# Kernel optimization log

Measured on AMD Instinct MI355X. Metric: run time of the kernel, lower is better.

The kernel has to match this reference:

```python
import jax, jax.numpy as jnp
import numpy as np

H = 4      # num_attention_heads
DK = 75    # d_k = hidden_size // H
HID = 300  # hidden_size


def setup_inputs() -> dict:
    key = jax.random.key(0)
    ks = jax.random.split(key, 9)
    B, S = 8, 2048
    query = jax.random.normal(ks[0], (B, S, HID), dtype=jnp.float32)
    key_t = jax.random.normal(ks[1], (B, S, HID), dtype=jnp.float32)
    value = jax.random.normal(ks[2], (B, S, HID), dtype=jnp.float32)
    mask = jax.random.randint(ks[3], (B, S), 0, 2, dtype=jnp.int32)
    scale = 1.0 / np.sqrt(HID)
    Wq = jax.random.normal(ks[4], (HID, HID), dtype=jnp.float32) * scale
    Wk = jax.random.normal(ks[5], (HID, HID), dtype=jnp.float32) * scale
    Wv = jax.random.normal(ks[6], (HID, HID), dtype=jnp.float32) * scale
    Wo = jax.random.normal(ks[7], (HID, HID), dtype=jnp.float32) * scale
    bo = jax.random.normal(ks[8], (HID,), dtype=jnp.float32) * 0.01
    return {"query": query, "key": key_t, "value": value, "mask": mask,
            "Wq": Wq, "Wk": Wk, "Wv": Wv, "Wo": Wo, "bo": bo}


def reference(query, key, value, mask, Wq, Wk, Wv, Wo, bo):
    B, S, _ = query.shape
    # QKV projections (nn.Linear: x @ W.T), split into heads: [B,H,S,DK]
    def proj(x, W):
        return (x @ W.T).reshape(B, S, H, DK).transpose(0, 2, 1, 3)
    q, k, v = proj(query, Wq), proj(key, Wk), proj(value, Wv)
    # scores: [B,H,S,S]
    scores = jnp.einsum('bhqd,bhkd->bhqk', q, k) / jnp.sqrt(jnp.float32(DK))
    # mask outer product 'bi,bj->bij' broadcast over heads; fill zeros with -1e9
    m2 = (mask[:, :, None] * mask[:, None, :])[:, None, :, :]  # [B,1,S,S]
    scores = jnp.where(m2 == 0, jnp.float32(-1e9), scores)
    p_attn = jax.nn.softmax(scores, axis=-1)  # dropout p=0.0 (eval mode)
    x = jnp.einsum('bhqk,bhkd->bhqd', p_attn, v)  # [B,H,S,DK]
    x = x.transpose(0, 2, 1, 3).reshape(B, S, H * DK)
    return x @ Wo.T + bo
```

## Files before the change

### kernel.cpp

```cpp
#include <hip/hip_runtime.h>
#include <math.h>

typedef __bf16 bf16x8 __attribute__((ext_vector_type(8)));
typedef float f32x4 __attribute__((ext_vector_type(4)));
typedef float f32x16 __attribute__((ext_vector_type(16)));
typedef unsigned short u16;
typedef u16 u16x8 __attribute__((ext_vector_type(8)));

#define HID 300
#define NH 4
#define DK 75
#define DKP 80
#define BB 8
#define SS 2048
#define BSROWS (BB*SS)
#define C2   0.16658807f

#define MFMA(a,b,c)   __builtin_amdgcn_mfma_f32_16x16x32_bf16(a,b,c,0,0,0)
#define MFMA32(a,b,c) __builtin_amdgcn_mfma_f32_32x32x16_bf16(a,b,c,0,0,0)

static __device__ __forceinline__ void split2(float x, u16& hb, u16& lb) {
    const unsigned u = __float_as_uint(x);
    hb = (u16)(u >> 16);
    const float r = x - __uint_as_float(u & 0xffff0000u);
    lb = (u16)(__float_as_uint(r) >> 16);
}
static __device__ __forceinline__ void split2rne(float x, u16& hb, u16& lb) {
    const unsigned u = __float_as_uint(x);
    const unsigned uh = ((u + 0x7fffu + ((u >> 16) & 1u)) >> 16) << 16;
    hb = (u16)(uh >> 16);
    const float r = x - __uint_as_float(uh);
    lb = (u16)(__float_as_uint(r) >> 16);
}
static __device__ __forceinline__ unsigned pkbf(float a, float b) {
    const unsigned short ua = __builtin_bit_cast(unsigned short, (__bf16)a);
    const unsigned short ub = __builtin_bit_cast(unsigned short, (__bf16)b);
    return (unsigned)ua | ((unsigned)ub << 16);
}

__global__ __launch_bounds__(256)
void prep_w3(const float* __restrict__ Wq, const float* __restrict__ Wk,
             const float* __restrict__ Wv,
             u16* __restrict__ wph, u16* __restrict__ wpl)
{
    const int idx = blockIdx.x * 256 + threadIdx.x;
    if (idx >= 38400) return;
    const int c8 = idx % 40;
    int r = idx / 40;
    const int n = r % 80; r /= 80;
    const int h = r & 3;  r >>= 2;
    const int mat = r;
    const float* W = (mat == 0) ? Wq : (mat == 1) ? Wk : Wv;
    const int col0 = c8 * 8;
    float v[8];
#pragma unroll
    for (int j = 0; j < 8; ++j) v[j] = 0.f;
    if (n < DK) {
        const float* s = W + (size_t)(h * DK + n) * HID + col0;
        if (col0 + 8 <= HID) {
#pragma unroll
            for (int j = 0; j < 8; ++j) v[j] = s[j];
        } else {
#pragma unroll
            for (int j = 0; j < 8; ++j) v[j] = (col0 + j < HID) ? s[j] : 0.f;
        }
    }
    u16x8 hv, lv;
#pragma unroll
    for (int j = 0; j < 8; ++j) {
        u16 hb, lb;
        split2(v[j], hb, lb);
        hv[j] = hb; lv[j] = lb;
    }
    const size_t base = ((size_t)((mat * 4 + h) * 80 + n)) * 320 + col0;
    *(u16x8*)(wph + base) = hv;
    *(u16x8*)(wpl + base) = lv;
}

static __device__ __forceinline__ void gemm_body(
    char* smem, const float* __restrict__ A, const float* __restrict__ W,
    const u16* __restrict__ Wph, const u16* __restrict__ Wpl,
    const float* __restrict__ bias, u16* __restrict__ hiP, u16* __restrict__ loP,
    float* __restrict__ foutP, const int mode, const int bx, const int h,
    const int* __restrict__ pmask, const float scale, const int patch)
{
    u16* Ah = (u16*)smem;
    u16* Al = Ah + 128 * 40;
    u16* Wh = Al + 128 * 40;
    u16* Wl = Wh + 80 * 40;

    const int t = threadIdx.x;
    const int wv = t >> 6, l = t & 63, qc = l & 15, g = l >> 4;
    const int row0 = bx * 128;
    const int b = row0 >> 11;
    const int s0 = row0 & 2047;

    const f32x4 zf = {0.f, 0.f, 0.f, 0.f};
    f32x4 acc[2][5];
#pragma unroll
    for (int mt = 0; mt < 2; ++mt)
#pragma unroll
        for (int nt = 0; nt < 5; ++nt) acc[mt][nt] = zf;

    const int rA = t >> 1, halfA = t & 1;
    float4 aPf[4];
    u16x8 wPfH[2], wPfL[2];
    float4 wPf2[3];

    auto loadA = [&](int step) {
        const int k0 = step * 32 + halfA * 16;
        const float* src = A + (size_t)(row0 + rA) * HID + k0;
#pragma unroll
        for (int c4 = 0; c4 < 4; ++c4) {
            const int k = k0 + c4 * 4;
            float4 v;
            if (k + 4 <= HID) v = *(const float4*)(src + c4 * 4);
            else {
                v.x = (k + 0 < HID) ? src[c4 * 4 + 0] : 0.f;
                v.y = (k + 1 < HID) ? src[c4 * 4 + 1] : 0.f;
                v.z = (k + 2 < HID) ? src[c4 * 4 + 2] : 0.f;
                v.w = (k + 3 < HID) ? src[c4 * 4 + 3] : 0.f;
            }
            aPf[c4] = v;
        }
    };
    auto loadW = [&](int step) {
        const int k0 = step * 32;
        if (mode <= 1) {
#pragma unroll
            for (int j = 0; j < 2; ++j) {
                const int idx = j * 256 + t;
                if (idx < 320) {
                    const int n = idx >> 2, c = idx & 3;
                    const size_t wo = (size_t)(h * 80 + n) * 320 + k0 + c * 8;
                    wPfH[j] = *(const u16x8*)(Wph + wo);
                    wPfL[j] = *(const u16x8*)(Wpl + wo);
                }
            }
        } else {
#pragma unroll
            for (int j = 0; j < 3; ++j) {
                const int idx = j * 256 + t;
                if (idx < 640) {
                    const int n = idx >> 3, c = idx & 7;
                    const int k = k0 + c * 4;
                    float4 v = make_float4(0.f, 0.f, 0.f, 0.f);
                    if (n < DK) {
                        const float* src = W + (size_t)(h * DK + n) * HID + k;
                        if (k + 4 <= HID) v = *(const float4*)src;
                        else {
                            v.x = (k + 0 < HID) ? src[0] : 0.f;
                            v.y = (k + 1 < HID) ? src[1] : 0.f;
                            v.z = (k + 2 < HID) ? src[2] : 0.f;
                            v.w = (k + 3 < HID) ? src[3] : 0.f;
                        }
                    }
                    wPf2[j] = v;
                }
            }
        }
    };
    auto writeA = [&]() {
        u16* dh = Ah + rA * 40 + halfA * 16;
        u16* dl = Al + rA * 40 + halfA * 16;
#pragma unroll
        for (int c4 = 0; c4 < 4; ++c4) {
            ushort4 h4, l4;
            split2(aPf[c4].x, h4.x, l4.x);
            split2(aPf[c4].y, h4.y, l4.y);
            split2(aPf[c4].z, h4.z, l4.z);
            split2(aPf[c4].w, h4.w, l4.w);
            *(ushort4*)(dh + c4 * 4) = h4;
            *(ushort4*)(dl + c4 * 4) = l4;
        }
    };
    auto writeW = [&]() {
        if (mode <= 1) {
#pragma unroll
            for (int j = 0; j < 2; ++j) {
                const int idx = j * 256 + t;
                if (idx < 320) {
                    const int n = idx >> 2, c = idx & 3;
                    *(u16x8*)(Wh + n * 40 + c * 8) = wPfH[j];
                    *(u16x8*)(Wl + n * 40 + c * 8) = wPfL[j];
                }
            }
        } else {
#pragma unroll
            for (int j = 0; j < 3; ++j) {
                const int idx = j * 256 + t;
                if (idx < 640) {
                    const int n = idx >> 3, c = idx & 7;
                    ushort4 h4, l4;
                    split2(wPf2[j].x, h4.x, l4.x);
                    split2(wPf2[j].y, h4.y, l4.y);
                    split2(wPf2[j].z, h4.z, l4.z);
                    split2(wPf2[j].w, h4.w, l4.w);
                    *(ushort4*)(Wh + n * 40 + c * 4) = h4;
                    *(ushort4*)(Wl + n * 40 + c * 4) = l4;
                }
            }
        }
    };

    loadA(0);
    loadW(0);

    for (int step = 0; step < 10; ++step) {
        __syncthreads();
        writeA();
        writeW();
        __syncthreads();
        if (step < 9) {
            loadA(step + 1);
            loadW(step + 1);
        }
        bf16x8 ah[2], al2[2];
#pragma unroll
        for (int mt = 0; mt < 2; ++mt) {
            const int roff = (wv * 32 + mt * 16 + qc) * 40 + g * 8;
            ah[mt]  = *(const bf16x8*)(Ah + roff);
            al2[mt] = *(const bf16x8*)(Al + roff);
        }
#pragma unroll
        for (int nt = 0; nt < 5; ++nt) {
            const int woff = (nt * 16 + qc) * 40 + g * 8;
            const bf16x8 bh = *(const bf16x8*)(Wh + woff);
            const bf16x8 bl = *(const bf16x8*)(Wl + woff);
#pragma unroll
            for (int mt = 0; mt < 2; ++mt) {
                acc[mt][nt] = MFMA(ah[mt],  bh, acc[mt][nt]);
                acc[mt][nt] = MFMA(al2[mt], bh, acc[mt][nt]);
                acc[mt][nt] = MFMA(ah[mt],  bl, acc[mt][nt]);
            }
        }
    }
    __syncthreads();

    if (mode <= 1) {
        unsigned* epi = (unsigned*)smem;
#pragma unroll
        for (int mt = 0; mt < 2; ++mt)
#pragma unroll
            for (int nt = 0; nt < 5; ++nt)
#pragma unroll
                for (int r = 0; r < 4; ++r) {
                    u16 hb, lb;
                    split2rne(acc[mt][nt][r] * scale, hb, lb);
                    if (patch != 0 && nt == 4 && qc == 11) {
                        if (patch == 1) { hb = (u16)0x3F80; lb = 0; }
                        else {
                            const int sr = s0 + wv * 32 + mt * 16 + g * 4 + r;
                            hb = (pmask[b * SS + sr] != 0) ? (u16)0 : (u16)0xC320;
                            lb = 0;
                        }
                    }
                    epi[(wv * 32 + mt * 16 + g * 4 + r) * 84 + nt * 16 + qc] =
                        (unsigned)hb | ((unsigned)lb << 16);
                }
        __syncthreads();
        if (mode == 0) {
            const int r = t >> 1, half = t & 1;
            const unsigned* row = epi + r * 84 + half * 40;
            const size_t base = ((size_t)(b * NH + h) * SS + s0 + r) * DKP + half * 40;
            u16* dh = hiP + base;
#pragma unroll
            for (int i = 0; i < 5; ++i) {
                u16x8 hv, lv;
#pragma unroll
                for (int j = 0; j < 8; ++j) {
                    const unsigned u = row[i * 8 + j];
                    hv[j] = (u16)u; lv[j] = (u16)(u >> 16);
                }
                *(u16x8*)(dh + i * 8) = hv;
                if (loP) *(u16x8*)(loP + base + i * 8) = lv;
            }
        } else {
#pragma unroll
            for (int i = 0; i < 3; ++i) {
                const int idx = i * 256 + t;
                if (idx < 640) {
                    const int d = idx >> 3, sc = (idx & 7) * 16;
                    const size_t base = ((size_t)(b * NH + h) * DKP + d) * SS + s0 + sc;
                    u16* dh = hiP + base;
                    u16x8 h0, h1, l0, l1;
#pragma unroll
                    for (int j = 0; j < 8; ++j) {
                        unsigned u = epi[(sc + j) * 84 + d];
                        h0[j] = (u16)u; l0[j] = (u16)(u >> 16);
                        u = epi[(sc + 8 + j) * 84 + d];
                        h1[j] = (u16)u; l1[j] = (u16)(u >> 16);
                    }
                    *(u16x8*)dh = h0; *(u16x8*)(dh + 8) = h1;
                    if (loP) {
                        *(u16x8*)(loP + base) = l0;
                        *(u16x8*)(loP + base + 8) = l1;
                    }
                }
            }
        }
    } else {
        float* epf = (float*)smem;
#pragma unroll
        for (int mt = 0; mt < 2; ++mt)
#pragma unroll
            for (int nt = 0; nt < 5; ++nt)
#pragma unroll
                for (int r = 0; r < 4; ++r)
                    epf[(wv * 32 + mt * 16 + g * 4 + r) * 84 + nt * 16 + qc] = acc[mt][nt][r];
        __syncthreads();
        for (int i = 0; i < 38; ++i) {
            const int idx = i * 256 + t;
            if (idx < 128 * DK) {
                const int r = idx / DK, c = idx - r * DK;
                foutP[(size_t)(row0 + r) * HID + h * DK + c] = epf[r * 84 + c] + bias[h * DK + c];
            }
        }
    }
}

__global__ __launch_bounds__(256)
void proj3_gemm(const float* __restrict__ Aq, const float* __restrict__ Ak,
                const float* __restrict__ Av, const int* __restrict__ mask,
                const u16* __restrict__ wph, const u16* __restrict__ wpl,
                u16* __restrict__ qh, u16* __restrict__ ql,
                u16* __restrict__ kh, u16* __restrict__ vh)
{
    __shared__ char smem[43008];
    const int z = blockIdx.z;
    const float* A = (z == 0) ? Aq : (z == 1) ? Ak : Av;
    const size_t WMAT = (size_t)4 * 80 * 320;
    u16* hiP = (z == 0) ? qh : (z == 1) ? kh : vh;
    u16* loP = (z == 0) ? ql : nullptr;
    const int mode = (z == 2) ? 1 : 0;
    const float scale = (z == 0) ? C2 : 1.0f;
    const int patch = (z == 0) ? 1 : (z == 1) ? 2 : 0;
    gemm_body(smem, A, nullptr, wph + z * WMAT, wpl + z * WMAT,
              nullptr, hiP, loP, nullptr, mode, blockIdx.x, blockIdx.y,
              mask, scale, patch);
}

__global__ __launch_bounds__(256)
void out_gemm(const float* __restrict__ A, const float* __restrict__ W,
              const float* __restrict__ bias, float* __restrict__ out)
{
    __shared__ char smem[43008];
    gemm_body(smem, A, W, nullptr, nullptr, bias, nullptr, nullptr, out, 2,
              blockIdx.x, blockIdx.y, nullptr, 1.0f, 0);
}

__global__ __launch_bounds__(256, 2)
void attn_mfma32(const u16* __restrict__ qhi, const u16* __restrict__ qlo,
                 const u16* __restrict__ khi, const u16* __restrict__ vhi,
                 const int* __restrict__ mask, float* __restrict__ xout)
{
    __shared__ u16 KsH[2 * 8192];
    __shared__ u16 VsH[2 * 6144];
    __shared__ u16 Ps[4 * 2048];

    const int t = threadIdx.x;
    const int wv = t >> 6;
    const int l = t & 63;
    const int q = l & 31;
    const int hi = l >> 5;

    const int bx = blockIdx.x;
    const int xcd = bx & 7, idx = bx >> 3;
    const int bh = xcd * 4 + (idx & 3);
    const int qt = idx >> 2;
    const int b = bh >> 2;
    const int h = bh & 3;
    const int q0 = qt * 128;

    {
        const int rr = (t >> 4) & 15, o8 = t & 15;
        *(uint2*)(VsH + (80 + rr) * 64 + o8 * 4) = make_uint2(0u, 0u);
        *(uint2*)(VsH + 6144 + (80 + rr) * 64 + o8 * 4) = make_uint2(0u, 0u);
    }

    const size_t planeQK = (size_t)bh * (SS * DKP);
    const int qrow = q0 + wv * 32 + q;
    const int mq = (mask[b * SS + qrow] != 0);
    const u16x8 qm = (u16x8)(u16)(mq ? 0xFFFFu : 0u);

    bf16x8 Qh[5], Ql[5];
    {
        const u16* ph = qhi + planeQK + (size_t)qrow * DKP;
        const u16* pl = qlo + planeQK + (size_t)qrow * DKP;
#pragma unroll
        for (int ch = 0; ch < 5; ++ch) {
            u16x8 ua = *(const u16x8*)(ph + 16 * ch + 8 * hi) & qm;
            u16x8 ub = *(const u16x8*)(pl + 16 * ch + 8 * hi) & qm;
            Qh[ch] = *(bf16x8*)&ua;
            Ql[ch] = *(bf16x8*)&ub;
        }
    }

    const u16* kH = khi + planeQK;
    const u16* vH = vhi + (size_t)bh * (DKP * SS);
    u16* PsW = Ps + wv * 2048;

    int kOff[5], kLds[5], vOff[5], vLds[5];
#pragma unroll
    for (int i = 0; i < 5; ++i) {
        const int gi = t + i * 256;
        const int r = gi / 20, c8 = gi % 20;
        kOff[i] = r * 160 + c8 * 8;
        kLds[i] = r * 256 + ((c8 * 8) ^ ((r & 7) << 4));
        const int d = gi >> 4, cv = gi & 15;
        vOff[i] = d * 4096 + cv * 8;
        vLds[i] = d * 128 + ((cv * 8) ^ ((d & 7) << 4));
    }

    uint2 kr[5], vr[5];
#define LOADT(KT) do { _Pragma("unroll") \
    for (int i = 0; i < 5; ++i) { \
        kr[i] = *(const uint2*)((const char*)kH + (size_t)(KT) * 10240 + kOff[i]); \
        vr[i] = *(const uint2*)((const char*)vH + (size_t)(KT) * 128 + vOff[i]); \
    } } while (0)
#define WRITET(BUF) do { _Pragma("unroll") \
    for (int i = 0; i < 5; ++i) { \
        *(uint2*)((char*)(KsH + (BUF) * 8192) + kLds[i]) = kr[i]; \
        *(uint2*)((char*)(VsH + (BUF) * 6144) + vLds[i]) = vr[i]; \
    } } while (0)

    LOADT(0);
    WRITET(0);
    LOADT(1);
    __syncthreads();

    f32x16 O[3];
#pragma unroll
    for (int dt = 0; dt < 3; ++dt) O[dt] = (f32x16){};
    float ll = 0.f;
    const int kswz = (q & 7) << 4;
    const int pswz = kswz;

    for (int kt = 0; kt < 32; ++kt) {
        const int cur = kt & 1;
        const char* Kc = (const char*)(KsH + cur * 8192);
        const char* Vc = (const char*)(VsH + cur * 6144);

        f32x16 s0 = (f32x16){}, s1 = (f32x16){};
#pragma unroll
        for (int ch = 0; ch < 5; ++ch) {
            const int o = (32 * ch + 16 * hi) ^ kswz;
            const bf16x8 a0 = *(const bf16x8*)(Kc + q * 256 + o);
            const bf16x8 a1 = *(const bf16x8*)(Kc + (32 + q) * 256 + o);
            s0 = MFMA32(a0, Qh[ch], s0);
            s0 = MFMA32(a0, Ql[ch], s0);
            s1 = MFMA32(a1, Qh[ch], s1);
            s1 = MFMA32(a1, Ql[ch], s1);
        }

        float p0 = 0.f, p1 = 0.f, p2 = 0.f, p3 = 0.f;
#pragma unroll
        for (int sb = 0; sb < 2; ++sb) {
            const f32x16 sv = sb ? s1 : s0;
            float e[16];
#pragma unroll
            for (int r = 0; r < 16; r += 4) {
                e[r + 0] = __builtin_amdgcn_exp2f(sv[r + 0]);
                e[r + 1] = __builtin_amdgcn_exp2f(sv[r + 1]);
                e[r + 2] = __builtin_amdgcn_exp2f(sv[r + 2]);
                e[r + 3] = __builtin_amdgcn_exp2f(sv[r + 3]);
                p0 += e[r + 0]; p1 += e[r + 1]; p2 += e[r + 2]; p3 += e[r + 3];
            }
#pragma unroll
            for (int rr = 0; rr < 4; ++rr) {
                uint2 w;
                w.x = pkbf(e[4 * rr + 0], e[4 * rr + 1]);
                w.y = pkbf(e[4 * rr + 2], e[4 * rr + 3]);
                const int o = (sb * 64 + 16 * rr + 8 * hi) ^ pswz;
                *(uint2*)((char*)PsW + q * 128 + o) = w;
            }
        }
        ll += (p0 + p1) + (p2 + p3);

#pragma unroll
        for (int c = 0; c < 4; ++c) {
            const int po = q * 128 + ((32 * c + 16 * hi) ^ pswz);
            const bf16x8 pA = *(const bf16x8*)((char*)PsW + po);
#pragma unroll
            for (int dt = 0; dt < 3; ++dt) {
                const int drow = 32 * dt + q;
                const int vb = drow * 128 + ((32 * c + 16 * hi) ^ ((drow & 7) << 4));
                const bf16x8 vh8 = *(const bf16x8*)(Vc + vb);
                O[dt] = MFMA32(vh8, pA, O[dt]);
            }
        }

        if (kt < 31) {
            WRITET(cur ^ 1);
            if (kt < 30) LOADT(kt + 2);
        }
        __syncthreads();
    }
#undef LOADT
#undef WRITET

    ll += __shfl_xor(ll, 32);
    {
        const float inv = 1.0f / ll;
        float* o = xout + (size_t)(b * SS + qrow) * HID + h * DK;
#pragma unroll
        for (int dt = 0; dt < 3; ++dt)
#pragma unroll
            for (int r = 0; r < 16; ++r) {
                const int d = 32 * dt + (r & 3) + 8 * (r >> 2) + 4 * hi;
                if (d < DK) o[d] = O[dt][r] * inv;
            }
    }
}

extern "C" void kernel_launch(void* const* d_in, const int* in_sizes, int n_in,
                              void* d_out, int out_size, void* d_ws, size_t ws_size,
                              hipStream_t stream)
{
    const float* query = (const float*)d_in[0];
    const float* key_t = (const float*)d_in[1];
    const float* value = (const float*)d_in[2];
    const int*   mask  = (const int*)d_in[3];
    const float* Wq    = (const float*)d_in[4];
    const float* Wk    = (const float*)d_in[5];
    const float* Wv    = (const float*)d_in[6];
    const float* Wo    = (const float*)d_in[7];
    const float* bo    = (const float*)d_in[8];
    float* out = (float*)d_out;

    const size_t PL = (size_t)BB * NH * SS * DKP;
    u16* qh = (u16*)d_ws;
    u16* ql = qh + PL;
    u16* kh = ql + PL;
    u16* kl = kh + PL;   (void)kl;
    u16* vh = kl + PL;
    u16* vl = vh + PL;
    float* xws = (float*)(vl + PL);
    u16* wph = (u16*)xws;
    u16* wpl = wph + (size_t)3 * 4 * 80 * 320;

    const dim3 blk(256, 1, 1);

    prep_w3<<<150, blk, 0, stream>>>(Wq, Wk, Wv, wph, wpl);

    proj3_gemm<<<dim3(128, NH, 3), blk, 0, stream>>>(query, key_t, value, mask,
                                                     wph, wpl,
                                                     qh, ql, kh, vh);

    attn_mfma32<<<dim3(512, 1, 1), blk, 0, stream>>>(qh, ql, kh, vh, mask, xws);

    out_gemm<<<dim3(128, NH, 1), blk, 0, stream>>>(xws, Wo, bo, out);
}
```

Baseline: 179.2 us.

## Process two heads per block in QKV projection GEMM to reuse A tiles

```diff
diff --git a/kernel.cpp b/kernel.cpp
--- a/kernel.cpp
+++ b/kernel.cpp
@@ -77,17 +77,20 @@
     *(u16x8*)(wpl + base) = lv;
 }
 
+template <int MODE, int HPB>
 static __device__ __forceinline__ void gemm_body(
     char* smem, const float* __restrict__ A, const float* __restrict__ W,
     const u16* __restrict__ Wph, const u16* __restrict__ Wpl,
     const float* __restrict__ bias, u16* __restrict__ hiP, u16* __restrict__ loP,
-    float* __restrict__ foutP, const int mode, const int bx, const int h,
+    float* __restrict__ foutP, const int bx, const int hp,
     const int* __restrict__ pmask, const float scale, const int patch)
 {
+    constexpr int WROWS = 80 * HPB;
+    constexpr int NT = 5 * HPB;
     u16* Ah = (u16*)smem;
     u16* Al = Ah + 128 * 40;
     u16* Wh = Al + 128 * 40;
-    u16* Wl = Wh + 80 * 40;
+    u16* Wl = Wh + WROWS * 40;
 
     const int t = threadIdx.x;
     const int wv = t >> 6, l = t & 63, qc = l & 15, g = l >> 4;
@@ -96,16 +99,18 @@
     const int s0 = row0 & 2047;
 
     const f32x4 zf = {0.f, 0.f, 0.f, 0.f};
-    f32x4 acc[2][5];
+    f32x4 acc[2][NT];
 #pragma unroll
     for (int mt = 0; mt < 2; ++mt)
 #pragma unroll
-        for (int nt = 0; nt < 5; ++nt) acc[mt][nt] = zf;
+        for (int nt = 0; nt < NT; ++nt) acc[mt][nt] = zf;
 
     const int rA = t >> 1, halfA = t & 1;
     float4 aPf[4];
-    u16x8 wPfH[2], wPfL[2];
-    float4 wPf2[3];
+    constexpr int WJ  = (WROWS * 4 + 255) / 256;
+    constexpr int WJ2 = (WROWS * 8 + 255) / 256;
+    u16x8 wPfH[WJ], wPfL[WJ];
+    float4 wPf2[WJ2];
 
     auto loadA = [&](int step) {
         const int k0 = step * 32 + halfA * 16;
@@ -126,27 +131,29 @@
     };
     auto loadW = [&](int step) {
         const int k0 = step * 32;
-        if (mode <= 1) {
-#pragma unroll
-            for (int j = 0; j < 2; ++j) {
+        if constexpr (MODE <= 1) {
+#pragma unroll
+            for (int j = 0; j < WJ; ++j) {
                 const int idx = j * 256 + t;
-                if (idx < 320) {
+                if (idx < WROWS * 4) {
                     const int n = idx >> 2, c = idx & 3;
-                    const size_t wo = (size_t)(h * 80 + n) * 320 + k0 + c * 8;
+                    const int nh = (n >= 80) ? 1 : 0, nn = n - nh * 80;
+                    const size_t wo = (size_t)((hp * HPB + nh) * 80 + nn) * 320 + k0 + c * 8;
                     wPfH[j] = *(const u16x8*)(Wph + wo);
                     wPfL[j] = *(const u16x8*)(Wpl + wo);
                 }
             }
         } else {
 #pragma unroll
-            for (int j = 0; j < 3; ++j) {
+            for (int j = 0; j < WJ2; ++j) {
                 const int idx = j * 256 + t;
-                if (idx < 640) {
+                if (idx < WROWS * 8) {
                     const int n = idx >> 3, c = idx & 7;
+                    const int nh = (n >= 80) ? 1 : 0, nn = n - nh * 80;
                     const int k = k0 + c * 4;
                     float4 v = make_float4(0.f, 0.f, 0.f, 0.f);
-                    if (n < DK) {
-                        const float* src = W + (size_t)(h * DK + n) * HID + k;
+                    if (nn < DK) {
+                        const float* src = W + (size_t)((hp * HPB + nh) * DK + nn) * HID + k;
                         if (k + 4 <= HID) v = *(const float4*)src;
                         else {
                             v.x = (k + 0 < HID) ? src[0] : 0.f;
@@ -175,11 +182,11 @@
         }
     };
     auto writeW = [&]() {
-        if (mode <= 1) {
-#pragma unroll
-            for (int j = 0; j < 2; ++j) {
+        if constexpr (MODE <= 1) {
+#pragma unroll
+            for (int j = 0; j < WJ; ++j) {
                 const int idx = j * 256 + t;
-                if (idx < 320) {
+                if (idx < WROWS * 4) {
                     const int n = idx >> 2, c = idx & 3;
                     *(u16x8*)(Wh + n * 40 + c * 8) = wPfH[j];
                     *(u16x8*)(Wl + n * 40 + c * 8) = wPfL[j];
@@ -187,9 +194,9 @@
             }
         } else {
 #pragma unroll
-            for (int j = 0; j < 3; ++j) {
+            for (int j = 0; j < WJ2; ++j) {
                 const int idx = j * 256 + t;
-                if (idx < 640) {
+                if (idx < WROWS * 8) {
                     const int n = idx >> 3, c = idx & 7;
                     ushort4 h4, l4;
                     split2(wPf2[j].x, h4.x, l4.x);
@@ -223,7 +230,7 @@
             al2[mt] = *(const bf16x8*)(Al + roff);
         }
 #pragma unroll
-        for (int nt = 0; nt < 5; ++nt) {
+        for (int nt = 0; nt < NT; ++nt) {
             const int woff = (nt * 16 + qc) * 40 + g * 8;
             const bf16x8 bh = *(const bf16x8*)(Wh + woff);
             const bf16x8 bl = *(const bf16x8*)(Wl + woff);
@@ -237,107 +244,117 @@
     }
     __syncthreads();
 
-    if (mode <= 1) {
-        unsigned* epi = (unsigned*)smem;
-#pragma unroll
-        for (int mt = 0; mt < 2; ++mt)
-#pragma unroll
-            for (int nt = 0; nt < 5; ++nt)
-#pragma unroll
-                for (int r = 0; r < 4; ++r) {
-                    u16 hb, lb;
-                    split2rne(acc[mt][nt][r] * scale, hb, lb);
-                    if (patch != 0 && nt == 4 && qc == 11) {
-                        if (patch == 1) { hb = (u16)0x3F80; lb = 0; }
-                        else {
-                            const int sr = s0 + wv * 32 + mt * 16 + g * 4 + r;
-                            hb = (pmask[b * SS + sr] != 0) ? (u16)0 : (u16)0xC320;
-                            lb = 0;
+#pragma unroll
+    for (int ph = 0; ph < HPB; ++ph) {
+        const int h = hp * HPB + ph;
+        if constexpr (MODE <= 1) {
+            unsigned* epi = (unsigned*)smem;
+#pragma unroll
+            for (int mt = 0; mt < 2; ++mt)
+#pragma unroll
+                for (int nt = 0; nt < 5; ++nt)
+#pragma unroll
+                    for (int r = 0; r < 4; ++r) {
+                        u16 hb, lb;
+                        split2rne(acc[mt][ph * 5 + nt][r] * scale, hb, lb);
+                        if (patch != 0 && nt == 4 && qc == 11) {
+                            if (patch == 1) { hb = (u16)0x3F80; lb = 0; }
+                            else {
+                                const int sr = s0 + wv * 32 + mt * 16 + g * 4 + r;
+                                hb = (pmask[b * SS + sr] != 0) ? (u16)0 : (u16)0xC320;
+                                lb = 0;
+                            }
+                        }
+                        epi[(wv * 32 + mt * 16 + g * 4 + r) * 84 + nt * 16 + qc] =
+                            (unsigned)hb | ((unsigned)lb << 16);
+                    }
+            __syncthreads();
+            if constexpr (MODE == 0) {
+                const int r = t >> 1, half = t & 1;
+                const unsigned* row = epi + r * 84 + half * 40;
+                const size_t base = ((size_t)(b * NH + h) * SS + s0 + r) * DKP + half * 40;
+                u16* dh = hiP + base;
+#pragma unroll
+                for (int i = 0; i < 5; ++i) {
+                    u16x8 hv, lv;
+#pragma unroll
+                    for (int j = 0; j < 8; ++j) {
+                        const unsigned u = row[i * 8 + j];
+                        hv[j] = (u16)u; lv[j] = (u16)(u >> 16);
+                    }
+                    *(u16x8*)(dh + i * 8) = hv;
+                    if (loP) *(u16x8*)(loP + base + i * 8) = lv;
+                }
+            } else {
+#pragma unroll
+                for (int i = 0; i < 3; ++i) {
+                    const int idx = i * 256 + t;
+                    if (idx < 640) {
+                        const int d = idx >> 3, sc = (idx & 7) * 16;
+                        const size_t base = ((size_t)(b * NH + h) * DKP + d) * SS + s0 + sc;
+                        u16* dh = hiP + base;
+                        u16x8 h0, h1, l0, l1;
+#pragma unroll
+                        for (int j = 0; j < 8; ++j) {
+                            unsigned u = epi[(sc + j) * 84 + d];
+                            h0[j] = (u16)u; l0[j] = (u16)(u >> 16);
+                            u = epi[(sc + 8 + j) * 84 + d];
+                            h1[j] = (u16)u; l1[j] = (u16)(u >> 16);
+                        }
+                        *(u16x8*)dh = h0; *(u16x8*)(dh + 8) = h1;
+                        if (loP) {
+                            *(u16x8*)(loP + base) = l0;
+                            *(u16x8*)(loP + base + 8) = l1;
                         }
                     }
-                    epi[(wv * 32 + mt * 16 + g * 4 + r) * 84 + nt * 16 + qc] =
-                        (unsigned)hb | ((unsigned)lb << 16);
-                }
-        __syncthreads();
-        if (mode == 0) {
-            const int r = t >> 1, half = t & 1;
-            const unsigned* row = epi + r * 84 + half * 40;
-            const size_t base = ((size_t)(b * NH + h) * SS + s0 + r) * DKP + half * 40;
-            u16* dh = hiP + base;
-#pragma unroll
-            for (int i = 0; i < 5; ++i) {
-                u16x8 hv, lv;
-#pragma unroll
-                for (int j = 0; j < 8; ++j) {
-                    const unsigned u = row[i * 8 + j];
-                    hv[j] = (u16)u; lv[j] = (u16)(u >> 16);
-                }
-                *(u16x8*)(dh + i * 8) = hv;
-                if (loP) *(u16x8*)(loP + base + i * 8) = lv;
+                }
             }
         } else {
-#pragma unroll
-            for (int i = 0; i < 3; ++i) {
+            float* epf = (float*)smem;
+#pragma unroll
+            for (int mt = 0; mt < 2; ++mt)
+#pragma unroll
+                for (int nt = 0; nt < 5; ++nt)
+#pragma unroll
+                    for (int r = 0; r < 4; ++r)
+                        epf[(wv * 32 + mt * 16 + g * 4 + r) * 84 + nt * 16 + qc] =
+                            acc[mt][ph * 5 + nt][r];
+            __syncthreads();
+            for (int i = 0; i < 38; ++i) {
                 const int idx = i * 256 + t;
-                if (idx < 640) {
-                    const int d = idx >> 3, sc = (idx & 7) * 16;
-                    const size_t base = ((size_t)(b * NH + h) * DKP + d) * SS + s0 + sc;
-                    u16* dh = hiP + base;
-                    u16x8 h0, h1, l0, l1;
-#pragma unroll
-                    for (int j = 0; j < 8; ++j) {
-                        unsigned u = epi[(sc + j) * 84 + d];
-                        h0[j] = (u16)u; l0[j] = (u16)(u >> 16);
-                        u = epi[(sc + 8 + j) * 84 + d];
-                        h1[j] = (u16)u; l1[j] = (u16)(u >> 16);
-                    }
-                    *(u16x8*)dh = h0; *(u16x8*)(dh + 8) = h1;
-                    if (loP) {
-                        *(u16x8*)(loP + base) = l0;
-                        *(u16x8*)(loP + base + 8) = l1;
-                    }
-                }
-            }
-        }
-    } else {
-        float* epf = (float*)smem;
-#pragma unroll
-        for (int mt = 0; mt < 2; ++mt)
-#pragma unroll
-            for (int nt = 0; nt < 5; ++nt)
-#pragma unroll
-                for (int r = 0; r < 4; ++r)
-                    epf[(wv * 32 + mt * 16 + g * 4 + r) * 84 + nt * 16 + qc] = acc[mt][nt][r];
-        __syncthreads();
-        for (int i = 0; i < 38; ++i) {
-            const int idx = i * 256 + t;
-            if (idx < 128 * DK) {
-                const int r = idx / DK, c = idx - r * DK;
-                foutP[(size_t)(row0 + r) * HID + h * DK + c] = epf[r * 84 + c] + bias[h * DK + c];
-            }
-        }
-    }
-}
-
-__global__ __launch_bounds__(256)
+                if (idx < 128 * DK) {
+                    const int r = idx / DK, c = idx - r * DK;
+                    foutP[(size_t)(row0 + r) * HID + h * DK + c] = epf[r * 84 + c] + bias[h * DK + c];
+                }
+            }
+        }
+        if (ph + 1 < HPB) __syncthreads();
+    }
+}
+
+__global__ __launch_bounds__(256, 3)
 void proj3_gemm(const float* __restrict__ Aq, const float* __restrict__ Ak,
                 const float* __restrict__ Av, const int* __restrict__ mask,
                 const u16* __restrict__ wph, const u16* __restrict__ wpl,
                 u16* __restrict__ qh, u16* __restrict__ ql,
                 u16* __restrict__ kh, u16* __restrict__ vh)
 {
-    __shared__ char smem[43008];
+    __shared__ char smem[46080];
     const int z = blockIdx.z;
     const float* A = (z == 0) ? Aq : (z == 1) ? Ak : Av;
     const size_t WMAT = (size_t)4 * 80 * 320;
     u16* hiP = (z == 0) ? qh : (z == 1) ? kh : vh;
     u16* loP = (z == 0) ? ql : nullptr;
-    const int mode = (z == 2) ? 1 : 0;
     const float scale = (z == 0) ? C2 : 1.0f;
     const int patch = (z == 0) ? 1 : (z == 1) ? 2 : 0;
-    gemm_body(smem, A, nullptr, wph + z * WMAT, wpl + z * WMAT,
-              nullptr, hiP, loP, nullptr, mode, blockIdx.x, blockIdx.y,
-              mask, scale, patch);
+    if (z == 2)
+        gemm_body<1, 2>(smem, A, nullptr, wph + z * WMAT, wpl + z * WMAT,
+                        nullptr, hiP, loP, nullptr, blockIdx.x, blockIdx.y,
+                        mask, scale, patch);
+    else
+        gemm_body<0, 2>(smem, A, nullptr, wph + z * WMAT, wpl + z * WMAT,
+                        nullptr, hiP, loP, nullptr, blockIdx.x, blockIdx.y,
+                        mask, scale, patch);
 }
 
 __global__ __launch_bounds__(256)
@@ -345,8 +362,8 @@
               const float* __restrict__ bias, float* __restrict__ out)
 {
     __shared__ char smem[43008];
-    gemm_body(smem, A, W, nullptr, nullptr, bias, nullptr, nullptr, out, 2,
-              blockIdx.x, blockIdx.y, nullptr, 1.0f, 0);
+    gemm_body<2, 1>(smem, A, W, nullptr, nullptr, bias, nullptr, nullptr, out,
+                    blockIdx.x, blockIdx.y, nullptr, 1.0f, 0);
 }
 
 __global__ __launch_bounds__(256, 2)
@@ -543,9 +560,9 @@
 
     prep_w3<<<150, blk, 0, stream>>>(Wq, Wk, Wv, wph, wpl);
 
-    proj3_gemm<<<dim3(128, NH, 3), blk, 0, stream>>>(query, key_t, value, mask,
-                                                     wph, wpl,
-                                                     qh, ql, kh, vh);
+    proj3_gemm<<<dim3(128, 2, 3), blk, 0, stream>>>(query, key_t, value, mask,
+                                                    wph, wpl,
+                                                    qh, ql, kh, vh);
 
     attn_mfma32<<<dim3(512, 1, 1), blk, 0, stream>>>(qh, ql, kh, vh, mask, xws);
 
```

After: 174.1 us. 1.03x faster.
